# Kernel tuning notes

Hardware: AMD Instinct MI355X
Metric: run time of the kernel (lower is better)

Reference implementation:

```python
import jax, jax.numpy as jnp
import numpy as np
from jax import lax

THRESH = 0.6      # pnet score threshold (threshold[0])
IOU_THR = 0.5     # per-scale nms threshold in detect_face
K_PICKS = 128     # fixed max number of NMS picks (jit-static)
STRIDE = 2.0
CELL = 12.0
NEG = -1e30


def _conv(x, w, b):
    y = lax.conv_general_dilated(x, w, (1, 1), 'VALID',
                                 dimension_numbers=('NCHW', 'OIHW', 'NCHW'))
    return y + b[None, :, None, None]


def _prelu(x, a):
    return jnp.where(x > 0, x, a[None, :, None, None] * x)


def _maxpool2(x):
    return lax.reduce_window(x, -jnp.inf, lax.max, (1, 1, 2, 2), (1, 1, 2, 2), 'VALID')


def _nms(boxes, scores):
    # Greedy union-IoU NMS (nms_numpy math), vectorized with a fixed pick budget.
    # boxes [N,4] (shared grid), scores [N] with invalid entries already = NEG.
    x1, y1, x2, y2 = boxes[:, 0], boxes[:, 1], boxes[:, 2], boxes[:, 3]
    area = (x2 - x1 + 1.0) * (y2 - y1 + 1.0)

    def body(live, _):
        j = jnp.argmax(live)
        s = live[j]
        ok = s > NEG * 0.5
        xx1 = jnp.maximum(x1[j], x1); yy1 = jnp.maximum(y1[j], y1)
        xx2 = jnp.minimum(x2[j], x2); yy2 = jnp.minimum(y2[j], y2)
        inter = jnp.maximum(0.0, xx2 - xx1 + 1.0) * jnp.maximum(0.0, yy2 - yy1 + 1.0)
        iou = inter / (area[j] + area - inter)
        live = jnp.where(iou > IOU_THR, NEG, live).at[j].set(NEG)
        return live, (j, ok)

    _, (idx, ok) = lax.scan(body, scores, None, length=K_PICKS)
    return idx, ok


def setup_inputs():
    key = jax.random.key(0)
    ks = jax.random.split(key, 16)
    B, H, W = 16, 384, 512
    f = lambda k, shp, s=0.1: jax.random.normal(k, shp, jnp.float32) * s
    return {
        'im_data': jax.random.uniform(ks[0], (B, 3, H, W), jnp.float32) * 255.0,
        'c1_w': f(ks[1], (10, 3, 3, 3)), 'c1_b': f(ks[2], (10,)),
        'p1': jnp.full((10,), 0.25, jnp.float32),
        'c2_w': f(ks[3], (16, 10, 3, 3)), 'c2_b': f(ks[4], (16,)),
        'p2': jnp.full((16,), 0.25, jnp.float32),
        'c3_w': f(ks[5], (32, 16, 3, 3)), 'c3_b': f(ks[6], (32,)),
        'p3': jnp.full((32,), 0.25, jnp.float32),
        'c41_w': f(ks[7], (2, 32, 1, 1)), 'c41_b': f(ks[8], (2,)),
        'c42_w': f(ks[9], (4, 32, 1, 1)), 'c42_b': f(ks[10], (4,)),
    }


def reference(im_data, c1_w, c1_b, p1, c2_w, c2_b, p2, c3_w, c3_b, p3,
              c41_w, c41_b, c42_w, c42_b):
    # --- PNet conv trunk (detect_face normalization + MTCNN PNet) ---
    x = (im_data - 127.5) * 0.0078125
    h = _prelu(_conv(x, c1_w, c1_b), p1)
    h = _maxpool2(h)                                   # 2x2 s2 (dims even -> ceil==floor)
    h = _prelu(_conv(h, c2_w, c2_b), p2)
    h = _prelu(_conv(h, c3_w, c3_b), p3)
    probs = jax.nn.softmax(_conv(h, c41_w, c41_b), axis=1)[:, 1]   # [B,Hp,Wp]
    reg = _conv(h, c42_w, c42_b)                                   # [B,4,Hp,Wp]

    # --- generateBoundingBox (dense, masked instead of nonzero; scale=1) ---
    B, Hp, Wp = probs.shape
    yy, xx = jnp.meshgrid(jnp.arange(Hp, dtype=jnp.float32),
                          jnp.arange(Wp, dtype=jnp.float32), indexing='ij')
    boxes4 = jnp.stack([jnp.floor(STRIDE * xx + 1.0).ravel(),
                        jnp.floor(STRIDE * yy + 1.0).ravel(),
                        jnp.floor(STRIDE * xx + CELL).ravel(),
                        jnp.floor(STRIDE * yy + CELL).ravel()], axis=1)  # [N,4]
    scores = probs.reshape(B, -1)                                   # [B,N]
    regf = reg.reshape(B, 4, -1).transpose(0, 2, 1)                 # [B,N,4]
    masked = jnp.where(scores >= THRESH, scores, NEG)

    # --- per-image greedy NMS (batched_nms: images independent) ---
    idx, ok = jax.vmap(_nms, in_axes=(None, 0))(boxes4, masked)     # [B,K]
    pb = boxes4[idx]                                                # [B,K,4]
    ps = jnp.take_along_axis(scores, idx, axis=1)                   # [B,K]
    pr = jnp.take_along_axis(regf, idx[..., None], axis=1)          # [B,K,4]

    w = pb[..., 2] - pb[..., 0]
    hh = pb[..., 3] - pb[..., 1]
    q1 = pb[..., 0] + pr[..., 0] * w
    q2 = pb[..., 1] + pr[..., 1] * hh
    q3 = pb[..., 2] + pr[..., 2] * w
    q4 = pb[..., 3] + pr[..., 3] * hh
    rw = q3 - q1
    rh = q4 - q2
    l = jnp.maximum(rw, rh)
    nx1 = q1 + rw * 0.5 - l * 0.5
    ny1 = q2 + rh * 0.5 - l * 0.5
    out = jnp.stack([nx1, ny1, nx1 + l, ny1 + l, ps], axis=-1)      # [B,K,5]
    return out * ok[..., None].astype(out.dtype)
```

## Files before the change

kernel.cpp:

```cpp
#include <hip/hip_runtime.h>
#include <math.h>

#define BATCH 16
#define IH 384
#define IW 512
#define C1 10
#define P1H 191
#define P1W 255
#define C2 16
#define H2 189
#define W2 253
#define C3 32
#define H3 187
#define W3 251
#define N3 (H3*W3)
#define KP 128
#define CAP 7680
#define NEGV (-1e30f)

__global__ __launch_bounds__(256, 2) void k_conv1pool(
        const float* __restrict__ im, const float* __restrict__ w,
        const float* __restrict__ bia, const float* __restrict__ slope,
        float* __restrict__ outp) {
    int x = blockIdx.x * 16 + threadIdx.x;
    int y = blockIdx.y * 16 + threadIdx.y;
    int bb = blockIdx.z;
    if (x >= P1W || y >= P1H) return;

    float in[3][4][4];
    #pragma unroll
    for (int ci = 0; ci < 3; ++ci) {
        const float* p = im + (((size_t)bb * 3 + ci) * IH + 2 * y) * IW + 2 * x;
        #pragma unroll
        for (int r = 0; r < 4; ++r) {
            const float2* q = (const float2*)(p + (size_t)r * IW);
            float2 a0 = q[0], a1 = q[1];
            in[ci][r][0] = a0.x; in[ci][r][1] = a0.y;
            in[ci][r][2] = a1.x; in[ci][r][3] = a1.y;
        }
    }
    #pragma unroll
    for (int ci = 0; ci < 3; ++ci)
        #pragma unroll
        for (int r = 0; r < 4; ++r)
            #pragma unroll
            for (int c = 0; c < 4; ++c)
                in[ci][r][c] = (in[ci][r][c] - 127.5f) * 0.0078125f;

    #pragma unroll
    for (int oc = 0; oc < C1; ++oc) {
        const float* wo = w + oc * 27;
        float bv = bia[oc], sv = slope[oc];
        float best = -INFINITY;
        #pragma unroll
        for (int py = 0; py < 2; ++py)
            #pragma unroll
            for (int px = 0; px < 2; ++px) {
                float acc = bv;
                #pragma unroll
                for (int ci = 0; ci < 3; ++ci)
                    #pragma unroll
                    for (int ky = 0; ky < 3; ++ky)
                        #pragma unroll
                        for (int kx = 0; kx < 3; ++kx)
                            acc += in[ci][py + ky][px + kx] * wo[(ci * 3 + ky) * 3 + kx];
                float v = acc > 0.f ? acc : sv * acc;
                best = fmaxf(best, v);
            }
        outp[(((size_t)bb * C1 + oc) * P1H + y) * P1W + x] = best;
    }
}

__global__ __launch_bounds__(256, 2) void k_conv2(
        const float* __restrict__ inp, const float* __restrict__ w,
        const float* __restrict__ bia, const float* __restrict__ slope,
        float* __restrict__ outp) {
    int x0 = (blockIdx.x * 64 + threadIdx.x) * 2;
    int y  = blockIdx.y * 4 + threadIdx.y;
    int bb = blockIdx.z;
    if (x0 >= W2 || y >= H2) return;

    float a0[C2], a1[C2];
    #pragma unroll
    for (int oc = 0; oc < C2; ++oc) { a0[oc] = bia[oc]; a1[oc] = bia[oc]; }

    bool tail = (x0 + 3 > P1W - 1);

    for (int ci = 0; ci < C1; ++ci) {
        const float* p = inp + (((size_t)bb * C1 + ci) * P1H + y) * P1W + x0;
        float v[3][4];
        #pragma unroll
        for (int r = 0; r < 3; ++r) {
            const float* pr = p + (size_t)r * P1W;
            v[r][0] = pr[0]; v[r][1] = pr[1]; v[r][2] = pr[2];
            v[r][3] = tail ? 0.f : pr[3];
        }
        const float* wc = w + ci * 9;
        #pragma unroll
        for (int oc = 0; oc < C2; ++oc) {
            const float* wo = wc + oc * (C1 * 9);
            float s0 = a0[oc], s1 = a1[oc];
            #pragma unroll
            for (int ky = 0; ky < 3; ++ky)
                #pragma unroll
                for (int kx = 0; kx < 3; ++kx) {
                    float wv = wo[ky * 3 + kx];
                    s0 += v[ky][kx]     * wv;
                    s1 += v[ky][kx + 1] * wv;
                }
            a0[oc] = s0; a1[oc] = s1;
        }
    }
    bool px1 = (x0 + 1 < W2);
    #pragma unroll
    for (int oc = 0; oc < C2; ++oc) {
        float sl = slope[oc];
        float* o = outp + (((size_t)bb * C2 + oc) * H2 + y) * W2 + x0;
        float u0 = a0[oc]; o[0] = u0 > 0.f ? u0 : sl * u0;
        if (px1) { float u1 = a1[oc]; o[1] = u1 > 0.f ? u1 : sl * u1; }
    }
}

__global__ __launch_bounds__(256, 2) void k_conv3heads(
        const float* __restrict__ inp, const float* __restrict__ w3,
        const float* __restrict__ b3, const float* __restrict__ s3,
        const float* __restrict__ w41, const float* __restrict__ b41,
        const float* __restrict__ w42, const float* __restrict__ b42,
        float* __restrict__ scores, float4* __restrict__ regf) {
    int x0 = (blockIdx.x * 64 + threadIdx.x) * 2;
    int y  = blockIdx.y * 4 + threadIdx.y;
    int bb = blockIdx.z;
    if (x0 >= W3 || y >= H3) return;

    float a0[C3], a1[C3];
    #pragma unroll
    for (int oc = 0; oc < C3; ++oc) { a0[oc] = b3[oc]; a1[oc] = b3[oc]; }

    bool tail = (x0 + 3 > W2 - 1);

    for (int ci = 0; ci < C2; ++ci) {
        const float* p = inp + (((size_t)bb * C2 + ci) * H2 + y) * W2 + x0;
        float v[3][4];
        #pragma unroll
        for (int r = 0; r < 3; ++r) {
            const float* pr = p + (size_t)r * W2;
            v[r][0] = pr[0]; v[r][1] = pr[1]; v[r][2] = pr[2];
            v[r][3] = tail ? 0.f : pr[3];
        }
        const float* wc = w3 + ci * 9;
        #pragma unroll
        for (int oc = 0; oc < C3; ++oc) {
            const float* wo = wc + oc * (C2 * 9);
            float s0 = a0[oc], s1 = a1[oc];
            #pragma unroll
            for (int ky = 0; ky < 3; ++ky)
                #pragma unroll
                for (int kx = 0; kx < 3; ++kx) {
                    float wv = wo[ky * 3 + kx];
                    s0 += v[ky][kx]     * wv;
                    s1 += v[ky][kx + 1] * wv;
                }
            a0[oc] = s0; a1[oc] = s1;
        }
    }
    #pragma unroll
    for (int oc = 0; oc < C3; ++oc) {
        float u0 = a0[oc], u1 = a1[oc], sl = s3[oc];
        a0[oc] = u0 > 0.f ? u0 : sl * u0;
        a1[oc] = u1 > 0.f ? u1 : sl * u1;
    }

    float l00 = b41[0], l01 = b41[1], l10 = b41[0], l11 = b41[1];
    #pragma unroll
    for (int c = 0; c < C3; ++c) {
        float w0 = w41[c], w1 = w41[C3 + c];
        l00 += a0[c] * w0; l01 += a0[c] * w1;
        l10 += a1[c] * w0; l11 += a1[c] * w1;
    }
    float m0 = fmaxf(l00, l01), m1 = fmaxf(l10, l11);
    float p0 = expf(l01 - m0) / (expf(l00 - m0) + expf(l01 - m0));
    float p1 = expf(l11 - m1) / (expf(l10 - m1) + expf(l11 - m1));

    float r00 = b42[0], r01 = b42[1], r02 = b42[2], r03 = b42[3];
    float r10 = b42[0], r11 = b42[1], r12 = b42[2], r13 = b42[3];
    #pragma unroll
    for (int c = 0; c < C3; ++c) {
        float w0 = w42[c], w1 = w42[C3 + c], w2 = w42[2 * C3 + c], w3v = w42[3 * C3 + c];
        r00 += a0[c] * w0; r01 += a0[c] * w1; r02 += a0[c] * w2; r03 += a0[c] * w3v;
        r10 += a1[c] * w0; r11 += a1[c] * w1; r12 += a1[c] * w2; r13 += a1[c] * w3v;
    }

    size_t n0 = (size_t)bb * N3 + y * W3 + x0;
    scores[n0] = (p0 >= 0.6f) ? p0 : NEGV;
    regf[n0]   = make_float4(r00, r01, r02, r03);
    if (x0 + 1 < W3) {
        scores[n0 + 1] = (p1 >= 0.6f) ? p1 : NEGV;
        regf[n0 + 1]   = make_float4(r10, r11, r12, r13);
    }
}

__global__ __launch_bounds__(1024) void k_nms(
        const float* __restrict__ scores, const float4* __restrict__ regf,
        float* __restrict__ outp) {
    __shared__ float s_score[CAP];
    __shared__ int   s_idx[CAP];
    __shared__ float r_s[16];
    __shared__ int   r_i[16];
    __shared__ float s_picks[KP];
    __shared__ int   s_picki[KP];
    __shared__ int   s_misc[4];

    int tid = threadIdx.x;
    int bb = blockIdx.x;
    const float* sc = scores + (size_t)bb * N3;

    if (tid < 4) s_misc[tid] = 0;
    __syncthreads();

    int cnt = 0;
    for (int i = tid; i < N3; i += 1024) if (sc[i] > 0.f) cnt++;
    atomicAdd(&s_misc[0], cnt);
    __syncthreads();
    int M = s_misc[0];

    int cutbin = 0;
    if (M > CAP) {
        for (int i = tid; i < 2048; i += 1024) s_idx[i] = 0;
        __syncthreads();
        for (int i = tid; i < N3; i += 1024) {
            float s = sc[i];
            if (s > 0.f) {
                int b = (int)((s - 0.6f) * 5120.f);
                b = b < 0 ? 0 : (b > 2047 ? 2047 : b);
                atomicAdd(&s_idx[b], 1);
            }
        }
        __syncthreads();
        if (tid == 0) {
            int accum = 0, b = 2047;
            for (; b >= 0; --b) {
                int c = s_idx[b];
                if (accum + c > CAP) break;
                accum += c;
            }
            s_misc[2] = b + 1;
        }
        __syncthreads();
        cutbin = s_misc[2];
        __syncthreads();
    }

    for (int i = tid; i < N3; i += 1024) {
        float s = sc[i];
        if (s > 0.f) {
            bool keep = true;
            if (M > CAP) {
                int b = (int)((s - 0.6f) * 5120.f);
                b = b < 0 ? 0 : (b > 2047 ? 2047 : b);
                keep = (b >= cutbin);
            }
            if (keep) {
                int pos = atomicAdd(&s_misc[1], 1);
                if (pos < CAP) { s_score[pos] = s; s_idx[pos] = i; }
            }
        }
    }
    __syncthreads();
    int M2 = s_misc[1]; if (M2 > CAP) M2 = CAP;

    int np = 0;
    for (int pick = 0; pick < KP; ++pick) {
        float bs = -INFINITY; int bi = 0x7fffffff;
        for (int i = tid; i < M2; i += 1024) {
            float s = s_score[i]; int id = s_idx[i];
            if (s > bs || (s == bs && id < bi)) { bs = s; bi = id; }
        }
        #pragma unroll
        for (int off = 32; off; off >>= 1) {
            float os = __shfl_down(bs, off);
            int   oi = __shfl_down(bi, off);
            if (os > bs || (os == bs && oi < bi)) { bs = os; bi = oi; }
        }
        int lane = tid & 63, wv = tid >> 6;
        if (lane == 0) { r_s[wv] = bs; r_i[wv] = bi; }
        __syncthreads();
        if (tid == 0) {
            float ps = r_s[0]; int pi = r_i[0];
            for (int k = 1; k < 16; ++k) {
                float os = r_s[k]; int oi = r_i[k];
                if (os > ps || (os == ps && oi < pi)) { ps = os; pi = oi; }
            }
            s_picks[pick] = ps; s_picki[pick] = pi;
            r_s[0] = ps; r_i[0] = pi;
        }
        __syncthreads();
        float ps = r_s[0]; int pi = r_i[0];
        if (ps < 0.f) break;
        np = pick + 1;

        int pcx = pi % W3, pcy = pi / W3;
        float px1 = (float)(2 * pcx + 1), py1 = (float)(2 * pcy + 1);
        float px2 = (float)(2 * pcx + 12), py2 = (float)(2 * pcy + 12);
        for (int i = tid; i < M2; i += 1024) {
            float s = s_score[i];
            if (s > NEGV * 0.5f) {
                int id = s_idx[i];
                int cx = id % W3, cy = id / W3;
                float x1 = (float)(2 * cx + 1), y1 = (float)(2 * cy + 1);
                float x2 = (float)(2 * cx + 12), y2 = (float)(2 * cy + 12);
                float xx1 = fmaxf(px1, x1), yy1 = fmaxf(py1, y1);
                float xx2 = fminf(px2, x2), yy2 = fminf(py2, y2);
                float inter = fmaxf(0.f, xx2 - xx1 + 1.f) * fmaxf(0.f, yy2 - yy1 + 1.f);
                float iou = inter / (288.f - inter);
                if (iou > 0.5f) s_score[i] = NEGV;
            }
        }
        __syncthreads();
    }

    if (tid < KP) {
        float* o = outp + ((size_t)bb * KP + tid) * 5;
        if (tid < np) {
            int pi = s_picki[tid]; float ps = s_picks[tid];
            int cx = pi % W3, cy = pi / W3;
            float x1 = (float)(2 * cx + 1), y1 = (float)(2 * cy + 1);
            float x2 = (float)(2 * cx + 12), y2 = (float)(2 * cy + 12);
            float4 r = regf[(size_t)bb * N3 + pi];
            float wd = x2 - x1, hh = y2 - y1;
            float q1 = x1 + r.x * wd, q2 = y1 + r.y * hh;
            float q3 = x2 + r.z * wd, q4 = y2 + r.w * hh;
            float rw = q3 - q1, rh = q4 - q2;
            float L = fmaxf(rw, rh);
            float nx1 = q1 + rw * 0.5f - L * 0.5f;
            float ny1 = q2 + rh * 0.5f - L * 0.5f;
            o[0] = nx1; o[1] = ny1; o[2] = nx1 + L; o[3] = ny1 + L; o[4] = ps;
        } else {
            o[0] = 0.f; o[1] = 0.f; o[2] = 0.f; o[3] = 0.f; o[4] = 0.f;
        }
    }
}

extern "C" void kernel_launch(void* const* d_in, const int* in_sizes, int n_in,
                              void* d_out, int out_size, void* d_ws, size_t ws_size,
                              hipStream_t stream) {
    const float* im   = (const float*)d_in[0];
    const float* c1w  = (const float*)d_in[1];
    const float* c1b  = (const float*)d_in[2];
    const float* p1   = (const float*)d_in[3];
    const float* c2w  = (const float*)d_in[4];
    const float* c2b  = (const float*)d_in[5];
    const float* p2   = (const float*)d_in[6];
    const float* c3w  = (const float*)d_in[7];
    const float* c3b  = (const float*)d_in[8];
    const float* p3   = (const float*)d_in[9];
    const float* c41w = (const float*)d_in[10];
    const float* c41b = (const float*)d_in[11];
    const float* c42w = (const float*)d_in[12];
    const float* c42b = (const float*)d_in[13];

    float* ws = (float*)d_ws;
    const size_t POOL1_FLOATS = (size_t)BATCH * C1 * P1H * P1W;
    float*  pool1  = ws;
    float*  conv2b = ws + POOL1_FLOATS;
    float*  scoresb = ws;
    float4* regfb   = (float4*)(ws + (size_t)BATCH * N3);

    k_conv1pool<<<dim3(16, 12, BATCH), dim3(16, 16), 0, stream>>>(im, c1w, c1b, p1, pool1);
    k_conv2   <<<dim3(2, 48, BATCH), dim3(64, 4), 0, stream>>>(pool1, c2w, c2b, p2, conv2b);
    k_conv3heads<<<dim3(2, 47, BATCH), dim3(64, 4), 0, stream>>>(conv2b, c3w, c3b, p3,
                                                                 c41w, c41b, c42w, c42b,
                                                                 scoresb, regfb);
    k_nms<<<dim3(BATCH), dim3(1024), 0, stream>>>(scoresb, regfb, (float*)d_out);
}
```

Baseline: 269.4 us.

## Run conv3 on MFMA with split-fp16 operands and NHWC conv2 output

Rewrites the third convolution as an implicit GEMM on 32x32x16 fp16 MFMA instructions. To keep close to fp32 accuracy, both weights and activations are split into high and low fp16 parts and three MFMAs are summed per tile. The conv2 output is switched to a channel-last layout so each pixel's 16 channels load as vectors into LDS tiles, and a small prep kernel pre-splits the weights into the output buffer as scratch. The cost is an extra launch, a larger LDS footprint, and a small precision loss from dropping the low-low product term.

```diff
diff --git a/kernel.cpp b/kernel.cpp
--- a/kernel.cpp
+++ b/kernel.cpp
@@ -18,6 +18,13 @@
 #define CAP 7680
 #define NEGV (-1e30f)
 
+typedef _Float16 f16x8 __attribute__((ext_vector_type(8)));
+typedef _Float16 f16x4 __attribute__((ext_vector_type(4)));
+typedef float    f32x16 __attribute__((ext_vector_type(16)));
+
+#define PXT 98
+#define NSUB 3
+
 __global__ __launch_bounds__(256, 2) void k_conv1pool(
         const float* __restrict__ im, const float* __restrict__ w,
         const float* __restrict__ bia, const float* __restrict__ slope,
@@ -111,91 +118,171 @@
             a0[oc] = s0; a1[oc] = s1;
         }
     }
-    bool px1 = (x0 + 1 < W2);
     #pragma unroll
     for (int oc = 0; oc < C2; ++oc) {
         float sl = slope[oc];
-        float* o = outp + (((size_t)bb * C2 + oc) * H2 + y) * W2 + x0;
-        float u0 = a0[oc]; o[0] = u0 > 0.f ? u0 : sl * u0;
-        if (px1) { float u1 = a1[oc]; o[1] = u1 > 0.f ? u1 : sl * u1; }
-    }
-}
-
-__global__ __launch_bounds__(256, 2) void k_conv3heads(
-        const float* __restrict__ inp, const float* __restrict__ w3,
+        float u0 = a0[oc]; a0[oc] = u0 > 0.f ? u0 : sl * u0;
+        float u1 = a1[oc]; a1[oc] = u1 > 0.f ? u1 : sl * u1;
+    }
+    float* o = outp + (((size_t)bb * H2 + y) * W2 + x0) * C2;
+    float4* o4 = (float4*)o;
+    o4[0] = make_float4(a0[0],  a0[1],  a0[2],  a0[3]);
+    o4[1] = make_float4(a0[4],  a0[5],  a0[6],  a0[7]);
+    o4[2] = make_float4(a0[8],  a0[9],  a0[10], a0[11]);
+    o4[3] = make_float4(a0[12], a0[13], a0[14], a0[15]);
+    if (x0 + 1 < W2) {
+        float4* p4 = (float4*)(o + C2);
+        p4[0] = make_float4(a1[0],  a1[1],  a1[2],  a1[3]);
+        p4[1] = make_float4(a1[4],  a1[5],  a1[6],  a1[7]);
+        p4[2] = make_float4(a1[8],  a1[9],  a1[10], a1[11]);
+        p4[3] = make_float4(a1[12], a1[13], a1[14], a1[15]);
+    }
+}
+
+__global__ __launch_bounds__(256) void k_prep(const float* __restrict__ w3,
+                                              _Float16* __restrict__ wbuf) {
+    for (int e = threadIdx.x; e < 4608; e += 256) {
+        int oc = e / 144;
+        int rem = e - oc * 144;
+        int ic = rem / 9;
+        int tap = rem - ic * 9;
+        float v = w3[e];
+        _Float16 h = (_Float16)v;
+        _Float16 l = (_Float16)(v - (float)h);
+        int d = (tap * 32 + oc) * 16 + ic;
+        wbuf[d] = h;
+        wbuf[4608 + d] = l;
+    }
+}
+
+__global__ __launch_bounds__(256, 2) void k_conv3mfma(
+        const float* __restrict__ act,
+        const _Float16* __restrict__ wbuf,
         const float* __restrict__ b3, const float* __restrict__ s3,
         const float* __restrict__ w41, const float* __restrict__ b41,
         const float* __restrict__ w42, const float* __restrict__ b42,
         float* __restrict__ scores, float4* __restrict__ regf) {
-    int x0 = (blockIdx.x * 64 + threadIdx.x) * 2;
-    int y  = blockIdx.y * 4 + threadIdx.y;
+    __shared__ __align__(16) _Float16 Whl[2 * 4608];
+    __shared__ __align__(16) _Float16 Ah[6 * PXT * 16];
+    __shared__ __align__(16) _Float16 Al[6 * PXT * 16];
+    __shared__ __align__(16) float    htab[32 * 8];
+
+    int tid = threadIdx.x;
+    int bx = blockIdx.x * (NSUB * 32);
+    int by = blockIdx.y * 4;
     int bb = blockIdx.z;
-    if (x0 >= W3 || y >= H3) return;
-
-    float a0[C3], a1[C3];
-    #pragma unroll
-    for (int oc = 0; oc < C3; ++oc) { a0[oc] = b3[oc]; a1[oc] = b3[oc]; }
-
-    bool tail = (x0 + 3 > W2 - 1);
-
-    for (int ci = 0; ci < C2; ++ci) {
-        const float* p = inp + (((size_t)bb * C2 + ci) * H2 + y) * W2 + x0;
-        float v[3][4];
-        #pragma unroll
-        for (int r = 0; r < 3; ++r) {
-            const float* pr = p + (size_t)r * W2;
-            v[r][0] = pr[0]; v[r][1] = pr[1]; v[r][2] = pr[2];
-            v[r][3] = tail ? 0.f : pr[3];
-        }
-        const float* wc = w3 + ci * 9;
-        #pragma unroll
-        for (int oc = 0; oc < C3; ++oc) {
-            const float* wo = wc + oc * (C2 * 9);
-            float s0 = a0[oc], s1 = a1[oc];
+
+    {
+        const float4* src = (const float4*)wbuf;
+        float4* dst = (float4*)Whl;
+        for (int i = tid; i < 1152; i += 256) dst[i] = src[i];
+    }
+    {
+        int oc = tid >> 3, f = tid & 7;
+        float v;
+        if      (f == 0) v = b3[oc];
+        else if (f == 1) v = s3[oc];
+        else if (f == 2) v = w41[oc];
+        else if (f == 3) v = w41[32 + oc];
+        else             v = w42[(f - 4) * 32 + oc];
+        htab[tid] = v;
+    }
+    {
+        const float* actb = act + (size_t)bb * H2 * W2 * C2;
+        for (int e = tid; e < 6 * PXT * 4; e += 256) {
+            int ic4 = e & 3;
+            int t = e >> 2;
+            int px = t % PXT;
+            int row = t / PXT;
+            int yg = by + row, xg = bx + px;
+            float4 v = make_float4(0.f, 0.f, 0.f, 0.f);
+            if (yg < H2 && xg < W2)
+                v = *(const float4*)(actb + ((size_t)yg * W2 + xg) * C2 + ic4 * 4);
+            float xs0 = v.x, xs1 = v.y, xs2 = v.z, xs3 = v.w;
+            f16x4 hv, lv;
+            _Float16 h;
+            h = (_Float16)xs0; hv[0] = h; lv[0] = (_Float16)(xs0 - (float)h);
+            h = (_Float16)xs1; hv[1] = h; lv[1] = (_Float16)(xs1 - (float)h);
+            h = (_Float16)xs2; hv[2] = h; lv[2] = (_Float16)(xs2 - (float)h);
+            h = (_Float16)xs3; hv[3] = h; lv[3] = (_Float16)(xs3 - (float)h);
+            int d = (row * PXT + px) * 16 + ic4 * 4;
+            *(f16x4*)(Ah + d) = hv;
+            *(f16x4*)(Al + d) = lv;
+        }
+    }
+    __syncthreads();
+
+    int wv = tid >> 6, lane = tid & 63;
+    int col = lane & 31, half = lane >> 5, kg8 = half * 8;
+    int y = by + wv;
+    if (y >= H3) return;
+
+    f32x16 acc[NSUB];
+    #pragma unroll
+    for (int s = 0; s < NSUB; ++s)
+        #pragma unroll
+        for (int i = 0; i < 16; ++i) acc[s][i] = 0.f;
+
+    #pragma unroll
+    for (int ky = 0; ky < 3; ++ky) {
+        const _Float16* arh = Ah + (wv + ky) * (PXT * 16);
+        const _Float16* arl = Al + (wv + ky) * (PXT * 16);
+        #pragma unroll
+        for (int kx = 0; kx < 3; ++kx) {
+            int tap = ky * 3 + kx;
+            f16x8 wh = *(const f16x8*)(Whl + (tap * 32 + col) * 16 + kg8);
+            f16x8 wl = *(const f16x8*)(Whl + 4608 + (tap * 32 + col) * 16 + kg8);
             #pragma unroll
-            for (int ky = 0; ky < 3; ++ky)
-                #pragma unroll
-                for (int kx = 0; kx < 3; ++kx) {
-                    float wv = wo[ky * 3 + kx];
-                    s0 += v[ky][kx]     * wv;
-                    s1 += v[ky][kx + 1] * wv;
-                }
-            a0[oc] = s0; a1[oc] = s1;
-        }
-    }
-    #pragma unroll
-    for (int oc = 0; oc < C3; ++oc) {
-        float u0 = a0[oc], u1 = a1[oc], sl = s3[oc];
-        a0[oc] = u0 > 0.f ? u0 : sl * u0;
-        a1[oc] = u1 > 0.f ? u1 : sl * u1;
-    }
-
-    float l00 = b41[0], l01 = b41[1], l10 = b41[0], l11 = b41[1];
-    #pragma unroll
-    for (int c = 0; c < C3; ++c) {
-        float w0 = w41[c], w1 = w41[C3 + c];
-        l00 += a0[c] * w0; l01 += a0[c] * w1;
-        l10 += a1[c] * w0; l11 += a1[c] * w1;
-    }
-    float m0 = fmaxf(l00, l01), m1 = fmaxf(l10, l11);
-    float p0 = expf(l01 - m0) / (expf(l00 - m0) + expf(l01 - m0));
-    float p1 = expf(l11 - m1) / (expf(l10 - m1) + expf(l11 - m1));
-
-    float r00 = b42[0], r01 = b42[1], r02 = b42[2], r03 = b42[3];
-    float r10 = b42[0], r11 = b42[1], r12 = b42[2], r13 = b42[3];
-    #pragma unroll
-    for (int c = 0; c < C3; ++c) {
-        float w0 = w42[c], w1 = w42[C3 + c], w2 = w42[2 * C3 + c], w3v = w42[3 * C3 + c];
-        r00 += a0[c] * w0; r01 += a0[c] * w1; r02 += a0[c] * w2; r03 += a0[c] * w3v;
-        r10 += a1[c] * w0; r11 += a1[c] * w1; r12 += a1[c] * w2; r13 += a1[c] * w3v;
-    }
-
-    size_t n0 = (size_t)bb * N3 + y * W3 + x0;
-    scores[n0] = (p0 >= 0.6f) ? p0 : NEGV;
-    regf[n0]   = make_float4(r00, r01, r02, r03);
-    if (x0 + 1 < W3) {
-        scores[n0 + 1] = (p1 >= 0.6f) ? p1 : NEGV;
-        regf[n0 + 1]   = make_float4(r10, r11, r12, r13);
+            for (int s = 0; s < NSUB; ++s) {
+                int p = s * 32 + col + kx;
+                f16x8 bh = *(const f16x8*)(arh + p * 16 + kg8);
+                f16x8 bl = *(const f16x8*)(arl + p * 16 + kg8);
+                acc[s] = __builtin_amdgcn_mfma_f32_32x32x16_f16(wh, bh, acc[s], 0, 0, 0);
+                acc[s] = __builtin_amdgcn_mfma_f32_32x32x16_f16(wl, bh, acc[s], 0, 0, 0);
+                acc[s] = __builtin_amdgcn_mfma_f32_32x32x16_f16(wh, bl, acc[s], 0, 0, 0);
+            }
+        }
+    }
+
+    float L0[NSUB], L1[NSUB], R0[NSUB], R1[NSUB], R2[NSUB], R3[NSUB];
+    #pragma unroll
+    for (int s = 0; s < NSUB; ++s) { L0[s]=0.f; L1[s]=0.f; R0[s]=0.f; R1[s]=0.f; R2[s]=0.f; R3[s]=0.f; }
+
+    #pragma unroll
+    for (int r = 0; r < 16; ++r) {
+        int oc = (r & 3) + 8 * (r >> 2) + 4 * half;
+        float4 t0 = *(const float4*)&htab[oc * 8];
+        float4 t1 = *(const float4*)&htab[oc * 8 + 4];
+        #pragma unroll
+        for (int s = 0; s < NSUB; ++s) {
+            float v = acc[s][r] + t0.x;
+            v = v > 0.f ? v : v * t0.y;
+            L0[s] += v * t0.z; L1[s] += v * t0.w;
+            R0[s] += v * t1.x; R1[s] += v * t1.y;
+            R2[s] += v * t1.z; R3[s] += v * t1.w;
+        }
+    }
+
+    float hb0 = b41[0], hb1 = b41[1];
+    float rb0 = b42[0], rb1 = b42[1], rb2 = b42[2], rb3 = b42[3];
+
+    #pragma unroll
+    for (int s = 0; s < NSUB; ++s) {
+        float l0 = L0[s] + __shfl_xor(L0[s], 32) + hb0;
+        float l1 = L1[s] + __shfl_xor(L1[s], 32) + hb1;
+        float r0 = R0[s] + __shfl_xor(R0[s], 32) + rb0;
+        float r1 = R1[s] + __shfl_xor(R1[s], 32) + rb1;
+        float r2 = R2[s] + __shfl_xor(R2[s], 32) + rb2;
+        float r3 = R3[s] + __shfl_xor(R3[s], 32) + rb3;
+        float m = fmaxf(l0, l1);
+        float e0 = expf(l0 - m), e1 = expf(l1 - m);
+        float p = e1 / (e0 + e1);
+        int px = bx + s * 32 + col;
+        if (half == 0 && px < W3) {
+            size_t n = (size_t)bb * N3 + (size_t)y * W3 + px;
+            scores[n] = (p >= 0.6f) ? p : NEGV;
+            regf[n] = make_float4(r0, r1, r2, r3);
+        }
     }
 }
 
@@ -364,11 +451,13 @@
     float*  conv2b = ws + POOL1_FLOATS;
     float*  scoresb = ws;
     float4* regfb   = (float4*)(ws + (size_t)BATCH * N3);
-
+    _Float16* wbuf = (_Float16*)d_out;
+
+    k_prep<<<dim3(1), dim3(256), 0, stream>>>(c3w, wbuf);
     k_conv1pool<<<dim3(16, 12, BATCH), dim3(16, 16), 0, stream>>>(im, c1w, c1b, p1, pool1);
     k_conv2   <<<dim3(2, 48, BATCH), dim3(64, 4), 0, stream>>>(pool1, c2w, c2b, p2, conv2b);
-    k_conv3heads<<<dim3(2, 47, BATCH), dim3(64, 4), 0, stream>>>(conv2b, c3w, c3b, p3,
-                                                                 c41w, c41b, c42w, c42b,
-                                                                 scoresb, regfb);
+    k_conv3mfma<<<dim3(3, 47, BATCH), dim3(256), 0, stream>>>(conv2b, wbuf, c3b, p3,
+                                                              c41w, c41b, c42w, c42b,
+                                                              scoresb, regfb);
     k_nms<<<dim3(BATCH), dim3(1024), 0, stream>>>(scoresb, regfb, (float*)d_out);
 }
```

Result: faster. 244.8 us (-9.1%).
